# Kernel tuning notes

Measured on AMD Instinct MI355X. Metric: run time of the kernel, lower is better.

The kernel has to match this reference:

```python
import jax, jax.numpy as jnp
import numpy as np

DEG = 7
RANK = 8
B = 2_000_000

def setup_inputs() -> dict:
    key = jax.random.key(0)
    k_x, k0, k1, k2, k3 = jax.random.split(key, 5)
    d1 = DEG + 1
    # xavier_normal std = sqrt(2 / (fan_in + fan_out)); for 3D cores torch uses
    # fan_in = rank*(deg+1) style flattening, but any gaussian init is fine for a
    # numerical reference; use std matching 2D xavier on the (first, last) dims.
    def xavier(k, shape):
        fan_in, fan_out = shape[0], shape[-1]
        std = np.sqrt(2.0 / (fan_in + fan_out))
        return jax.random.normal(k, shape, dtype=jnp.float32) * std
    return {
        "X": jax.random.normal(k_x, (B, 4), dtype=jnp.float32),
        "G0": xavier(k0, (d1, RANK)),
        "G1": xavier(k1, (RANK, d1, RANK)),
        "G2": xavier(k2, (RANK, d1, RANK)),
        "G3": xavier(k3, (RANK, d1)),
    }

def reference(X, G0, G1, G2, G3):
    # poly bases: P[b, dim, p] = X[b, dim] ** p, p = 0..deg
    exps = jnp.arange(DEG + 1)               # [d1]
    P = X[:, :, None] ** exps                # [B, 4, d1]
    # chained TT contraction, left to right (avoids any large intermediate)
    t = jnp.einsum('bd,dr->br', P[:, 0], G0)           # [B, r]
    t = jnp.einsum('br,rds,bd->bs', t, G1, P[:, 1])    # [B, r]
    t = jnp.einsum('bs,sdt,bd->bt', t, G2, P[:, 2])    # [B, r]
    res = jnp.einsum('bt,td,bd->b', t, G3, P[:, 3])    # [B]
    return res.reshape(-1, 1)
```

## Files before the change

kernel.cpp:

```cpp
#include <hip/hip_runtime.h>
#include <hip/hip_bf16.h>

typedef float f32x4 __attribute__((ext_vector_type(4)));
typedef short bf16x8 __attribute__((ext_vector_type(8)));

__device__ inline unsigned cvt_pk_bf16(float a, float b) {
    unsigned r;
    asm("v_cvt_pk_bf16_f32 %0, %1, %2" : "=v"(r) : "v"(a), "v"(b));
    return r;
}
union FragU { unsigned u[4]; bf16x8 v; };

__device__ inline bf16x8 pack8(const float* f) {
    FragU x;
    x.u[0] = cvt_pk_bf16(f[0], f[1]);
    x.u[1] = cvt_pk_bf16(f[2], f[3]);
    x.u[2] = cvt_pk_bf16(f[4], f[5]);
    x.u[3] = cvt_pk_bf16(f[6], f[7]);
    return x.v;
}

__device__ inline void split_hl(const float* v, bf16x8& h8, bf16x8& l8) {
    float hi[8], lo[8];
    #pragma unroll
    for (int e = 0; e < 8; ++e) {
        float h = __bfloat162float(__float2bfloat16(v[e]));
        hi[e] = h; lo[e] = v[e] - h;
    }
    h8 = pack8(hi); l8 = pack8(lo);
}

__device__ inline float bperm_f(int idx_bytes, float v) {
    return __int_as_float(__builtin_amdgcn_ds_bpermute(idx_bytes, __float_as_int(v)));
}
__device__ inline float swz16_f(float v) {
    return __int_as_float(__builtin_amdgcn_ds_swizzle(__float_as_int(v), 0x401F));
}

#define POWERS(p, xx)                                              \
    p[0] = 1.f;  p[1] = (xx);      p[2] = p[1]*p[1];               \
    p[3] = p[2]*p[1]; p[4] = p[2]*p[2]; p[5] = p[4]*p[1];          \
    p[6] = p[4]*p[2]; p[7] = p[4]*p[3];

#define MFMA __builtin_amdgcn_mfma_f32_16x16x32_bf16

__global__ __launch_bounds__(256, 2) void tt_poly_kernel(
    const float* __restrict__ X,
    const float* __restrict__ G0,
    const float* __restrict__ G1,
    const float* __restrict__ G2,
    const float* __restrict__ G3,
    float* __restrict__ out,
    int B, int NW)
{
    const int tid   = threadIdx.x;
    const int lane  = tid & 63;
    const int row16 = lane & 15;
    const int quad  = lane >> 4;
    const int s8    = row16 & 7;
    const int gw    = blockIdx.x * 4 + (tid >> 6);

    float4 xva[4];
    #pragma unroll
    for (int it = 0; it < 4; ++it) {
        int b = (it * NW + gw) * 64 + lane;
        xva[it] = (b < B) ? reinterpret_cast<const float4*>(X)[b]
                          : make_float4(0.f, 0.f, 0.f, 0.f);
    }

    bf16x8 A1h[2], A1l[2], A2h[2], A2l[2], A3h[2], A3l[2];
    #pragma unroll
    for (int q = 0; q < 2; ++q) {
        float v[8];
        #pragma unroll
        for (int e = 0; e < 8; ++e) {
            float a = 0.f;
            #pragma unroll
            for (int r = 0; r < 8; ++r)
                a = fmaf(G0[e*8 + r], G1[(r*8 + 4*q + quad)*8 + s8], a);
            v[e] = a;
        }
        split_hl(v, A1h[q], A1l[q]);
    }
    #pragma unroll
    for (int q = 0; q < 2; ++q) {
        float v[8];
        #pragma unroll
        for (int e = 0; e < 8; ++e)
            v[e] = G2[(e*8 + 4*q + quad)*8 + s8];
        split_hl(v, A2h[q], A2l[q]);
    }
    #pragma unroll
    for (int q = 0; q < 2; ++q) {
        float v[8];
        #pragma unroll
        for (int e = 0; e < 8; ++e)
            v[e] = G3[e*8 + 4*q + quad];
        split_hl(v, A3h[q], A3l[q]);
    }

    const bool oddq  = (quad & 1) != 0;
    const float zero = 0.f;

    #pragma unroll
    for (int it = 0; it < 4; ++it) {
        const int sbase = (it * NW + gw) * 64;
        const float4 xv = xva[it];
        float res = 0.f;

        #pragma unroll
        for (int g4 = 0; g4 < 4; ++g4) {
            const int src = (g4 * 16 + row16) * 4;
            float x0 = bperm_f(src, xv.x);
            float x1 = bperm_f(src, xv.y);
            float x2 = bperm_f(src, xv.z);
            float x3 = bperm_f(src, xv.w);

            float p0[8];
            POWERS(p0, x0)
            float x1sq = x1 * x1, x1q4 = x1sq * x1sq;
            float sA = ((quad & 1) ? x1 : 1.f) * ((quad & 2) ? x1sq : 1.f);
            float sB = sA * x1q4;
            float f0[8], f1[8];
            #pragma unroll
            for (int e = 0; e < 8; ++e) { f0[e] = p0[e] * sA; f1[e] = p0[e] * sB; }
            bf16x8 b0 = pack8(f0), b1 = pack8(f1);
            f32x4 acc = {zero, zero, zero, zero};
            acc = MFMA(A1h[0], b0, acc, 0, 0, 0);
            acc = MFMA(A1l[0], b0, acc, 0, 0, 0);
            acc = MFMA(A1h[1], b1, acc, 0, 0, 0);
            acc = MFMA(A1l[1], b1, acc, 0, 0, 0);

            float t1v[8];
            {
                float sw0 = swz16_f(acc[0]), sw1 = swz16_f(acc[1]);
                float sw2 = swz16_f(acc[2]), sw3 = swz16_f(acc[3]);
                t1v[0] = oddq ? sw0 : acc[0];  t1v[4] = oddq ? acc[0] : sw0;
                t1v[1] = oddq ? sw1 : acc[1];  t1v[5] = oddq ? acc[1] : sw1;
                t1v[2] = oddq ? sw2 : acc[2];  t1v[6] = oddq ? acc[2] : sw2;
                t1v[3] = oddq ? sw3 : acc[3];  t1v[7] = oddq ? acc[3] : sw3;
            }

            float x2sq = x2 * x2, x2q4 = x2sq * x2sq;
            float uA = ((quad & 1) ? x2 : 1.f) * ((quad & 2) ? x2sq : 1.f);
            float uB = uA * x2q4;
            #pragma unroll
            for (int e = 0; e < 8; ++e) { f0[e] = t1v[e] * uA; f1[e] = t1v[e] * uB; }
            b0 = pack8(f0); b1 = pack8(f1);
            f32x4 acc2 = {zero, zero, zero, zero};
            acc2 = MFMA(A2h[0], b0, acc2, 0, 0, 0);
            acc2 = MFMA(A2l[0], b0, acc2, 0, 0, 0);
            acc2 = MFMA(A2h[1], b1, acc2, 0, 0, 0);
            acc2 = MFMA(A2l[1], b1, acc2, 0, 0, 0);

            float t2v[8];
            {
                float sw0 = swz16_f(acc2[0]), sw1 = swz16_f(acc2[1]);
                float sw2 = swz16_f(acc2[2]), sw3 = swz16_f(acc2[3]);
                t2v[0] = oddq ? sw0 : acc2[0];  t2v[4] = oddq ? acc2[0] : sw0;
                t2v[1] = oddq ? sw1 : acc2[1];  t2v[5] = oddq ? acc2[1] : sw1;
                t2v[2] = oddq ? sw2 : acc2[2];  t2v[6] = oddq ? acc2[2] : sw2;
                t2v[3] = oddq ? sw3 : acc2[3];  t2v[7] = oddq ? acc2[3] : sw3;
            }

            float x3sq = x3 * x3, x3q4 = x3sq * x3sq;
            float wA = ((quad & 1) ? x3 : 1.f) * ((quad & 2) ? x3sq : 1.f);
            float wB = wA * x3q4;
            #pragma unroll
            for (int e = 0; e < 8; ++e) { f0[e] = t2v[e] * wA; f1[e] = t2v[e] * wB; }
            b0 = pack8(f0); b1 = pack8(f1);
            f32x4 acc3 = {zero, zero, zero, zero};
            acc3 = MFMA(A3h[0], b0, acc3, 0, 0, 0);
            acc3 = MFMA(A3l[0], b0, acc3, 0, 0, 0);
            acc3 = MFMA(A3h[1], b1, acc3, 0, 0, 0);
            acc3 = MFMA(A3l[1], b1, acc3, 0, 0, 0);

            res = (quad == g4) ? acc3[0] : res;
        }

        const int b = sbase + lane;
        if (b < B) out[b] = res;
    }
}

extern "C" void kernel_launch(void* const* d_in, const int* in_sizes, int n_in,
                              void* d_out, int out_size, void* d_ws, size_t ws_size,
                              hipStream_t stream) {
    const float* X  = (const float*)d_in[0];
    const float* G0 = (const float*)d_in[1];
    const float* G1 = (const float*)d_in[2];
    const float* G2 = (const float*)d_in[3];
    const float* G3 = (const float*)d_in[4];
    float* out = (float*)d_out;

    int B = in_sizes[0] / 4;
    int block = 256;
    int grid = (B + 1023) / 1024;
    int NW = grid * 4;
    tt_poly_kernel<<<grid, block, 0, stream>>>(X, G0, G1, G2, G3, out, B, NW);
}
```

Measured before the change: 40.89 us.

## Load X per sample group directly, split MFMA accumulators, raise occupancy

Each 16-sample group's X row is now loaded straight from global memory, replacing the upfront prefetch of all four iterations plus ds_bpermute broadcasts. The iteration loop is no longer unrolled and launch bounds ask for 4 blocks per SM, aiming to cut register pressure and raise occupancy. The hi and lo MFMA chains now use separate accumulators that are summed afterwards, breaking the serial dependency. The risk is redundant global loads (each X row is read by 4 quads) and less memory-latency hiding without the prefetch.

```diff
diff --git a/kernel.cpp b/kernel.cpp
--- a/kernel.cpp
+++ b/kernel.cpp
@@ -30,9 +30,6 @@
     h8 = pack8(hi); l8 = pack8(lo);
 }
 
-__device__ inline float bperm_f(int idx_bytes, float v) {
-    return __int_as_float(__builtin_amdgcn_ds_bpermute(idx_bytes, __float_as_int(v)));
-}
 __device__ inline float swz16_f(float v) {
     return __int_as_float(__builtin_amdgcn_ds_swizzle(__float_as_int(v), 0x401F));
 }
@@ -44,7 +41,7 @@
 
 #define MFMA __builtin_amdgcn_mfma_f32_16x16x32_bf16
 
-__global__ __launch_bounds__(256, 2) void tt_poly_kernel(
+__global__ __launch_bounds__(256, 4) void tt_poly_kernel(
     const float* __restrict__ X,
     const float* __restrict__ G0,
     const float* __restrict__ G1,
@@ -59,14 +56,6 @@
     const int quad  = lane >> 4;
     const int s8    = row16 & 7;
     const int gw    = blockIdx.x * 4 + (tid >> 6);
-
-    float4 xva[4];
-    #pragma unroll
-    for (int it = 0; it < 4; ++it) {
-        int b = (it * NW + gw) * 64 + lane;
-        xva[it] = (b < B) ? reinterpret_cast<const float4*>(X)[b]
-                          : make_float4(0.f, 0.f, 0.f, 0.f);
-    }
 
     bf16x8 A1h[2], A1l[2], A2h[2], A2l[2], A3h[2], A3l[2];
     #pragma unroll
@@ -99,37 +88,34 @@
         split_hl(v, A3h[q], A3l[q]);
     }
 
-    const bool oddq  = (quad & 1) != 0;
-    const float zero = 0.f;
+    const bool oddq = (quad & 1) != 0;
 
-    #pragma unroll
+    #pragma unroll 1
     for (int it = 0; it < 4; ++it) {
         const int sbase = (it * NW + gw) * 64;
-        const float4 xv = xva[it];
-        float res = 0.f;
+        float resg[4];
 
         #pragma unroll
         for (int g4 = 0; g4 < 4; ++g4) {
-            const int src = (g4 * 16 + row16) * 4;
-            float x0 = bperm_f(src, xv.x);
-            float x1 = bperm_f(src, xv.y);
-            float x2 = bperm_f(src, xv.z);
-            float x3 = bperm_f(src, xv.w);
+            const int sidx = sbase + g4 * 16 + row16;
+            float4 xs = (sidx < B) ? reinterpret_cast<const float4*>(X)[sidx]
+                                   : make_float4(0.f, 0.f, 0.f, 0.f);
 
             float p0[8];
-            POWERS(p0, x0)
-            float x1sq = x1 * x1, x1q4 = x1sq * x1sq;
-            float sA = ((quad & 1) ? x1 : 1.f) * ((quad & 2) ? x1sq : 1.f);
+            POWERS(p0, xs.x)
+            float x1sq = xs.y * xs.y, x1q4 = x1sq * x1sq;
+            float sA = ((quad & 1) ? xs.y : 1.f) * ((quad & 2) ? x1sq : 1.f);
             float sB = sA * x1q4;
             float f0[8], f1[8];
             #pragma unroll
             for (int e = 0; e < 8; ++e) { f0[e] = p0[e] * sA; f1[e] = p0[e] * sB; }
             bf16x8 b0 = pack8(f0), b1 = pack8(f1);
-            f32x4 acc = {zero, zero, zero, zero};
-            acc = MFMA(A1h[0], b0, acc, 0, 0, 0);
-            acc = MFMA(A1l[0], b0, acc, 0, 0, 0);
-            acc = MFMA(A1h[1], b1, acc, 0, 0, 0);
-            acc = MFMA(A1l[1], b1, acc, 0, 0, 0);
+            f32x4 ah = {0.f, 0.f, 0.f, 0.f}, al = {0.f, 0.f, 0.f, 0.f};
+            ah = MFMA(A1h[0], b0, ah, 0, 0, 0);
+            al = MFMA(A1l[0], b0, al, 0, 0, 0);
+            ah = MFMA(A1h[1], b1, ah, 0, 0, 0);
+            al = MFMA(A1l[1], b1, al, 0, 0, 0);
+            f32x4 acc = ah + al;
 
             float t1v[8];
             {
@@ -141,17 +127,18 @@
                 t1v[3] = oddq ? sw3 : acc[3];  t1v[7] = oddq ? acc[3] : sw3;
             }
 
-            float x2sq = x2 * x2, x2q4 = x2sq * x2sq;
-            float uA = ((quad & 1) ? x2 : 1.f) * ((quad & 2) ? x2sq : 1.f);
+            float x2sq = xs.z * xs.z, x2q4 = x2sq * x2sq;
+            float uA = ((quad & 1) ? xs.z : 1.f) * ((quad & 2) ? x2sq : 1.f);
             float uB = uA * x2q4;
             #pragma unroll
             for (int e = 0; e < 8; ++e) { f0[e] = t1v[e] * uA; f1[e] = t1v[e] * uB; }
             b0 = pack8(f0); b1 = pack8(f1);
-            f32x4 acc2 = {zero, zero, zero, zero};
-            acc2 = MFMA(A2h[0], b0, acc2, 0, 0, 0);
-            acc2 = MFMA(A2l[0], b0, acc2, 0, 0, 0);
-            acc2 = MFMA(A2h[1], b1, acc2, 0, 0, 0);
-            acc2 = MFMA(A2l[1], b1, acc2, 0, 0, 0);
+            f32x4 bh = {0.f, 0.f, 0.f, 0.f}, bl = {0.f, 0.f, 0.f, 0.f};
+            bh = MFMA(A2h[0], b0, bh, 0, 0, 0);
+            bl = MFMA(A2l[0], b0, bl, 0, 0, 0);
+            bh = MFMA(A2h[1], b1, bh, 0, 0, 0);
+            bl = MFMA(A2l[1], b1, bl, 0, 0, 0);
+            f32x4 acc2 = bh + bl;
 
             float t2v[8];
             {
@@ -163,23 +150,24 @@
                 t2v[3] = oddq ? sw3 : acc2[3];  t2v[7] = oddq ? acc2[3] : sw3;
             }
 
-            float x3sq = x3 * x3, x3q4 = x3sq * x3sq;
-            float wA = ((quad & 1) ? x3 : 1.f) * ((quad & 2) ? x3sq : 1.f);
+            float x3sq = xs.w * xs.w, x3q4 = x3sq * x3sq;
+            float wA = ((quad & 1) ? xs.w : 1.f) * ((quad & 2) ? x3sq : 1.f);
             float wB = wA * x3q4;
             #pragma unroll
             for (int e = 0; e < 8; ++e) { f0[e] = t2v[e] * wA; f1[e] = t2v[e] * wB; }
             b0 = pack8(f0); b1 = pack8(f1);
-            f32x4 acc3 = {zero, zero, zero, zero};
-            acc3 = MFMA(A3h[0], b0, acc3, 0, 0, 0);
-            acc3 = MFMA(A3l[0], b0, acc3, 0, 0, 0);
-            acc3 = MFMA(A3h[1], b1, acc3, 0, 0, 0);
-            acc3 = MFMA(A3l[1], b1, acc3, 0, 0, 0);
-
-            res = (quad == g4) ? acc3[0] : res;
+            f32x4 ch = {0.f, 0.f, 0.f, 0.f}, cl = {0.f, 0.f, 0.f, 0.f};
+            ch = MFMA(A3h[0], b0, ch, 0, 0, 0);
+            cl = MFMA(A3l[0], b0, cl, 0, 0, 0);
+            ch = MFMA(A3h[1], b1, ch, 0, 0, 0);
+            cl = MFMA(A3l[1], b1, cl, 0, 0, 0);
+            resg[g4] = ch[0] + cl[0];
         }
 
+        float rv = (quad & 2) ? ((quad & 1) ? resg[3] : resg[2])
+                              : ((quad & 1) ? resg[1] : resg[0]);
         const int b = sbase + lane;
-        if (b < B) out[b] = res;
+        if (b < B) out[b] = rv;
     }
 }
 
```

Result: slower. 45.40 us (+11.0%).
